# Optimization experiments

Hardware: AMD Instinct MI355X
Metric: run time of the kernel (lower is better)

The kernel has to match this reference:

```python
import jax, jax.numpy as jnp
import numpy as np
from jax import lax

ALPHA = 0.5
TEMPORAL_UNIT = 0


def setup_inputs() -> dict:
    key = jax.random.key(0)
    k1, k2, k3 = jax.random.split(key, 3)
    B, T, C = 16, 1024, 64
    z1 = jax.random.normal(k1, (B, T, C), dtype=jnp.float32)
    z2 = jax.random.normal(k2, (B, T, C), dtype=jnp.float32)
    # irregular timestamps, sorted within each sequence
    t = jnp.sort(jax.random.uniform(k3, (B, T), dtype=jnp.float32) * T, axis=1)
    return {"z1": z1, "z2": z2, "t": t}


def _instance_contrastive_loss_aug(z1, z2, t):
    B, T, C = z1.shape
    if B == 1:
        return jnp.asarray(0.0, z1.dtype)
    N = B * T
    tf = t.reshape(N)
    diff = jnp.abs(tf[:, None] - tf[None, :])                  # [N, N]
    seq = jnp.repeat(jnp.arange(B), T)                         # [N]
    same_seq = seq[:, None] == seq[None, :]
    # torch: diff[mask] += diff.max() + 0.001 (max of original diff)
    diff = jnp.where(same_seq, diff + (diff.max() + 0.001), diff)
    # B smallest per row -> top_k of negated values
    _, idx = lax.top_k(-diff, B)                               # [N, B]
    z1f = z1.reshape(N, C)
    z2f = z2.reshape(N, C)
    pos = jnp.sum(z1f * z2f, axis=-1, keepdims=True)           # [N, 1]
    neg11 = jnp.einsum('nc,nbc->nb', z1f, z1f[idx])            # [N, B]
    neg12 = jnp.einsum('nc,nbc->nb', z1f, z2f[idx])            # [N, B]
    logits = jnp.concatenate([pos, neg11, neg12], axis=1)      # [N, 1+2B]
    return -jax.nn.log_softmax(logits, axis=1)[:, 0].mean()


def _temporal_contrastive_loss(z1, z2):
    B, T, C = z1.shape
    if T == 1:
        return jnp.asarray(0.0, z1.dtype)
    z = jnp.concatenate([z1, z2], axis=1)                      # [B, 2T, C]
    sim = jnp.einsum('bic,bjc->bij', z, z)                     # [B, 2T, 2T]
    logits = jnp.tril(sim, -1)[:, :, :-1] + jnp.triu(sim, 1)[:, :, 1:]
    logp = jax.nn.log_softmax(logits, axis=-1)
    i = jnp.arange(T)
    return -(logp[:, i, T + i - 1].mean() + logp[:, T + i, i].mean()) / 2


def _hierarchical_loss(z1, z2, t, alpha, temporal_unit):
    B = z1.shape[0]
    loss = jnp.asarray(0.0, z1.dtype)
    d = 0
    while z1.shape[1] > 1:
        if alpha != 0:
            loss = loss + alpha * _instance_contrastive_loss_aug(z1, z2, t)
        if d >= temporal_unit and (1 - alpha) != 0:
            loss = loss + (1 - alpha) * _temporal_contrastive_loss(z1, z2)
        d += 1
        # pool timestamps by mean-of-2 (drop trailing odd element)
        if t.shape[1] % 2 != 0:
            t = t[:, :-1]
        t = t.reshape(B, -1, 2).mean(axis=2)
        # max_pool1d(kernel=2, stride=2) along time (floor -> truncate to even)
        Te = (z1.shape[1] // 2) * 2
        z1 = z1[:, :Te].reshape(B, -1, 2, z1.shape[-1]).max(axis=2)
        z2 = z2[:, :Te].reshape(B, -1, 2, z2.shape[-1]).max(axis=2)
    if z1.shape[1] == 1:
        if alpha != 0:
            loss = loss + alpha * _instance_contrastive_loss_aug(z1, z2, t)
        d += 1
    return loss / d


def reference(z1, z2, t):
    return _hierarchical_loss(z1, z2, t, ALPHA, TEMPORAL_UNIT)
```

## Files before the change

kernel.cpp:

```cpp
#include <hip/hip_runtime.h>
#include <hip/hip_bf16.h>
#include <math.h>

#define B_ 16
#define C_ 64
#define NEG_BIG (-1e30f)
#define POS_BIG (1e30f)

typedef __attribute__((ext_vector_type(8))) short bf16x8;
typedef __attribute__((ext_vector_type(4))) float f32x4;

__device__ __forceinline__ short f2bf(float x) {
  __hip_bfloat16 h = __float2bfloat16(x);
  return *reinterpret_cast<short*>(&h);
}

__device__ constexpr int kTS[10]   = {0, 512, 768, 896, 960, 992, 1008, 1024, 1040, 1056};
__device__ constexpr int kZOff[10] = {0, 2097152, 3145728, 3670016, 3932160, 4063232,
                                      4128768, 4161536, 4177920, 4186112};
__device__ constexpr int kIS[11] = {0, 256, 384, 448, 480, 496, 504, 508, 510, 511, 512};
__device__ constexpr int kO1[11] = {0, 0, 1056768, 1585152, 1849344, 1981440, 2047488,
                                    2080512, 2097024, 2105280, 2109408};
__device__ constexpr int kO2[11] = {0, 524288, 1318912, 1716224, 1914880, 2014208, 2063872,
                                    2088704, 2101120, 2107328, 2110432};
__device__ constexpr int kOT[11] = {0, 1048576, 1581056, 1847296, 1980416, 2046976, 2080256,
                                    2096896, 2105216, 2109376, 2111456};

__global__ __launch_bounds__(256) void convert0_kernel(
    const float* __restrict__ z1, const float* __restrict__ z2, short* __restrict__ zcb)
{
  int i = blockIdx.x * 256 + threadIdx.x;
  int n = i * 8;
  int b = n >> 16;
  float4 u1 = *(const float4*)(z1 + n), v1 = *(const float4*)(z1 + n + 4);
  float4 u2 = *(const float4*)(z2 + n), v2 = *(const float4*)(z2 + n + 4);
  bf16x8 f1, f2;
  f1[0]=f2bf(u1.x); f1[1]=f2bf(u1.y); f1[2]=f2bf(u1.z); f1[3]=f2bf(u1.w);
  f1[4]=f2bf(v1.x); f1[5]=f2bf(v1.y); f1[6]=f2bf(v1.z); f1[7]=f2bf(v1.w);
  f2[0]=f2bf(u2.x); f2[1]=f2bf(u2.y); f2[2]=f2bf(u2.z); f2[3]=f2bf(u2.w);
  f2[4]=f2bf(v2.x); f2[5]=f2bf(v2.y); f2[6]=f2bf(v2.z); f2[7]=f2bf(v2.w);
  *(bf16x8*)(zcb + (size_t)n + (size_t)b * 65536) = f1;
  *(bf16x8*)(zcb + (size_t)n + (size_t)(b + 1) * 65536) = f2;
}

__global__ __launch_bounds__(256) void downsample_kernel(
    const float* __restrict__ z1s, const float* __restrict__ z2s, const float* __restrict__ ts,
    float* __restrict__ z1d, float* __restrict__ z2d, float* __restrict__ td,
    short* __restrict__ zcb_l, int Td)
{
  int idx = blockIdx.x * blockDim.x + threadIdx.x;
  int total_z = B_ * Td * C_;
  if (idx < total_z) {
    int bi = idx >> 6;
    int b  = bi / Td;
    int s  = (b * (2 * Td) + 2 * (bi % Td)) * C_ + (idx & (C_ - 1));
    float v1 = fmaxf(z1s[s], z1s[s + C_]);
    float v2 = fmaxf(z2s[s], z2s[s + C_]);
    z1d[idx] = v1; z2d[idx] = v2;
    if (zcb_l) {
      int zi = idx + b * Td * C_;
      zcb_l[zi] = f2bf(v1);
      zcb_l[zi + Td * C_] = f2bf(v2);
    }
  } else {
    int k = idx - total_z;
    if (k < B_ * Td) {
      int i = k % Td, b = k / Td;
      int s = b * (2 * Td) + 2 * i;
      td[k] = 0.5f * (ts[s] + ts[s + 1]);
    }
  }
}

__global__ __launch_bounds__(256) void instance_fused(
    const float* __restrict__ z1_0, const float* __restrict__ z2_0, const float* __restrict__ t_0,
    const float* __restrict__ ws, float* __restrict__ out)
{
  __shared__ float dmin[64 * 17], dLl[64 * 17], dRl[64 * 17];
  __shared__ int   Lp[64 * 17], Rp[64 * 17];
  __shared__ int   nbrs[64][16];

  int bid = blockIdx.x;
  int l = 0, ls = 0;
  #pragma unroll
  for (int i = 1; i < 11; i++) if (bid >= kIS[i]) { l = i; ls = kIS[i]; }
  int T = 1024 >> l, lgT = 10 - l, N = B_ * T;
  const float *z1, *z2, *t;
  if (l == 0) { z1 = z1_0; z2 = z2_0; t = t_0; }
  else {
    int i1 = 0, i2 = 0, it = 0;
    #pragma unroll
    for (int i = 1; i < 11; i++) if (l == i) { i1 = kO1[i]; i2 = kO2[i]; it = kOT[i]; }
    z1 = ws + i1; z2 = ws + i2; t = ws + it;
  }
  float scale = 0.5f / (11.0f * (float)N);

  int tid = threadIdx.x;
  int rbase = (bid - ls) * 64;

  if (T == 1) {
    for (int idx = tid; idx < 64 * 16; idx += 256)
      nbrs[idx >> 4][idx & 15] = idx & 15;
  } else {
    for (int idx = tid; idx < 64 * 16; idx += 256) {
      int r = idx >> 4, s = idx & 15;
      int n = rbase + r;
      if (s < 15 && n < N) {
        int bq = n >> lgT;
        float q = t[n];
        int bs = s + (s >= bq ? 1 : 0);
        const float* tb = t + (bs << lgT);
        int li = 0;
        for (int k = T >> 1; k; k >>= 1) li += (tb[li + k - 1] < q) ? k : 0;
        li += (tb[li] < q) ? 1 : 0;
        float dl = (li >= 1) ? (q - tb[li - 1]) : POS_BIG;
        float dr = (li < T)  ? (tb[li] - q)     : POS_BIG;
        int o = r * 17 + s;
        Lp[o] = li - 1; Rp[o] = li;
        dLl[o] = dl; dRl[o] = dr; dmin[o] = fminf(dl, dr);
      }
    }
  }
  __syncthreads();

  int w = tid >> 6, lane = tid & 63;

  if (T > 1 && lane < 16) {
    int r = w * 16 + lane;
    int n = rbase + r;
    if (n < N) {
      int bq = n >> lgT;
      float q = t[n];
      #pragma unroll 1
      for (int j = 0; j < 16; j++) {
        float best = dmin[r * 17]; int sb = 0;
        #pragma unroll
        for (int s = 1; s < 15; s++) {
          float c = dmin[r * 17 + s];
          bool lt = c < best; best = lt ? c : best; sb = lt ? s : sb;
        }
        int o = r * 17 + sb;
        int bs = sb + (sb >= bq ? 1 : 0);
        float dl = dLl[o], dr = dRl[o];
        if (dl <= dr) {
          int p = Lp[o];
          nbrs[r][j] = bs * T + p;
          int pn = p - 1; Lp[o] = pn;
          float nd = (pn >= 0) ? (q - t[bs * T + pn]) : POS_BIG;
          dLl[o] = nd; dmin[o] = fminf(nd, dr);
        } else {
          int p = Rp[o];
          nbrs[r][j] = bs * T + p;
          int pn = p + 1; Rp[o] = pn;
          float nd = (pn < T) ? (t[bs * T + pn] - q) : POS_BIG;
          dRl[o] = nd; dmin[o] = fminf(dl, nd);
        }
      }
    } else {
      #pragma unroll
      for (int j = 0; j < 16; j++) nbrs[r][j] = 0;
    }
  }
  __syncthreads();

  int g = lane >> 4, sl = lane & 15;
  float loss = 0.f;
  #pragma unroll 1
  for (int rc = 0; rc < 4; rc++) {
    int r = w * 16 + rc * 4 + g;
    int n = rbase + r;
    bool act = n < N;
    int ns = act ? n : rbase;
    float4 za = *(const float4*)(z1 + (size_t)ns * C_ + sl * 4);
    float4 zp = *(const float4*)(z2 + (size_t)ns * C_ + sl * 4);
    float pos = za.x * zp.x + za.y * zp.y + za.z * zp.z + za.w * zp.w;
    float a11[16], a12[16];
    #pragma unroll
    for (int j = 0; j < 16; j++) {
      int nb = nbrs[r][j];
      float4 uu = *(const float4*)(z1 + (size_t)nb * C_ + sl * 4);
      float4 vv = *(const float4*)(z2 + (size_t)nb * C_ + sl * 4);
      a11[j] = za.x * uu.x + za.y * uu.y + za.z * uu.z + za.w * uu.w;
      a12[j] = za.x * vv.x + za.y * vv.y + za.z * vv.z + za.w * vv.w;
    }
    #pragma unroll
    for (int msk = 1; msk < 16; msk <<= 1) {
      pos += __shfl_xor(pos, msk, 16);
      #pragma unroll
      for (int j = 0; j < 16; j++) {
        a11[j] += __shfl_xor(a11[j], msk, 16);
        a12[j] += __shfl_xor(a12[j], msk, 16);
      }
    }
    if (sl == 0 && act) {
      float m = pos;
      #pragma unroll
      for (int j = 0; j < 16; j++) m = fmaxf(m, fmaxf(a11[j], a12[j]));
      float se = __expf(pos - m);
      #pragma unroll
      for (int j = 0; j < 16; j++) se += __expf(a11[j] - m) + __expf(a12[j] - m);
      loss += (m + __logf(se)) - pos;
    }
  }
  #pragma unroll
  for (int off = 32; off; off >>= 1) loss += __shfl_down(loss, off, 64);
  if (lane == 0) atomicAdd(out, loss * scale);
}

__global__ __launch_bounds__(256) void temporal_fused(
    const float* __restrict__ z1_0, const float* __restrict__ z2_0,
    const float* __restrict__ ws, const short* __restrict__ zcb, float* __restrict__ out)
{
  __shared__ __align__(16) short sb[64 * 64];

  int orig = blockIdx.x;
  int bid = (orig & 7) * 134 + (orig >> 3);

  int l = 0, ls = 0;
  #pragma unroll
  for (int i = 1; i < 10; i++) if (bid >= kTS[i]) { l = i; ls = kTS[i]; }
  int T = 1024 >> l, TT = 2 * T;
  int lb = bid - ls;
  int lg = (5 - l) > 0 ? (5 - l) : 0;
  int b = lb >> lg, rblk = lb & ((1 << lg) - 1);

  int zoff = 0, fo1 = 0, fo2 = 0;
  #pragma unroll
  for (int i = 1; i < 10; i++) if (l == i) { zoff = kZOff[i]; fo1 = kO1[i]; fo2 = kO2[i]; }
  const short* zl = zcb + zoff + (size_t)b * TT * C_;
  const float* z1b = ((l == 0) ? z1_0 : ws + fo1) + (size_t)b * T * C_;
  const float* z2b = ((l == 0) ? z2_0 : ws + fo2) + (size_t)b * T * C_;

  int tid = threadIdx.x;
  int wv = tid >> 6, lane = tid & 63, lo = lane & 15, hi = lane >> 4;
  int rowbase = rblk * 64 + wv * 16;
  bool activew = rowbase < TT;
  int diagch = rowbase >> 6;

  int ar = rowbase + lo; if (ar >= TT) ar = TT - 1;
  const short* pa = zl + (size_t)ar * C_;
  bf16x8 a0 = *(const bf16x8*)(pa + hi * 8);
  bf16x8 a1 = *(const bf16x8*)(pa + 32 + hi * 8);

  float m[4], s[4];
  #pragma unroll
  for (int sl = 0; sl < 4; sl++) { m[sl] = NEG_BIG; s[sl] = 0.f; }

  int c0 = tid, c1 = tid + 256;
  int r0 = c0 >> 3, s0 = c0 & 7, r1 = c1 >> 3, s1 = c1 & 7;
  int swb0 = r0 * 128 + ((s0 * 16) ^ ((r0 & 7) << 4));
  int swb1 = r1 * 128 + ((s1 * 16) ^ ((r1 & 7) << 4));

  int nch = (TT + 63) >> 6;
  int rr0 = r0, rr1 = r1;
  int q0 = rr0; if (q0 >= TT) q0 = TT - 1;
  int q1 = rr1; if (q1 >= TT) q1 = TT - 1;
  float4 st0 = *(const float4*)(zl + (size_t)q0 * C_ + s0 * 8);
  float4 st1 = *(const float4*)(zl + (size_t)q1 * C_ + s1 * 8);

  for (int ch = 0; ch < nch; ch++) {
    int cb = ch << 6;
    __syncthreads();
    *(float4*)((char*)sb + swb0) = st0;
    *(float4*)((char*)sb + swb1) = st1;
    __syncthreads();
    if (ch + 1 < nch) {
      int nb0 = cb + 64 + rr0; if (nb0 >= TT) nb0 = TT - 1;
      int nb1 = cb + 64 + rr1; if (nb1 >= TT) nb1 = TT - 1;
      st0 = *(const float4*)(zl + (size_t)nb0 * C_ + s0 * 8);
      st1 = *(const float4*)(zl + (size_t)nb1 * C_ + s1 * 8);
    }
    if (activew) {
      f32x4 acc[4];
      #pragma unroll
      for (int tt = 0; tt < 4; tt++) {
        int br = tt * 16 + lo;
        int byt = br * 128 + ((hi * 16) ^ ((br & 7) << 4));
        bf16x8 b0 = *(const bf16x8*)((const char*)sb + byt);
        bf16x8 b1 = *(const bf16x8*)((const char*)sb + (byt ^ 64));
        f32x4 c = {0.f, 0.f, 0.f, 0.f};
        c = __builtin_amdgcn_mfma_f32_16x16x32_bf16(a0, b0, c, 0, 0, 0);
        c = __builtin_amdgcn_mfma_f32_16x16x32_bf16(a1, b1, c, 0, 0, 0);
        acc[tt] = c;
      }
      bool maskpath = (ch == diagch) || (cb + 64 > TT);
      if (maskpath) {
        #pragma unroll
        for (int sl = 0; sl < 4; sl++) {
          int r = rowbase + hi * 4 + sl;
          float v[4]; float vmax = NEG_BIG;
          #pragma unroll
          for (int tt = 0; tt < 4; tt++) {
            int cg = cb + tt * 16 + lo;
            bool excl = (cg >= TT) || (cg == r);
            v[tt] = excl ? NEG_BIG : acc[tt][sl];
            vmax = fmaxf(vmax, v[tt]);
          }
          if (vmax > -1e29f) {
            float mn = fmaxf(m[sl], vmax);
            float ss = s[sl] * __expf(m[sl] - mn);
            #pragma unroll
            for (int tt = 0; tt < 4; tt++) ss += __expf(v[tt] - mn);
            s[sl] = ss; m[sl] = mn;
          }
        }
      } else {
        #pragma unroll
        for (int sl = 0; sl < 4; sl++) {
          float vmax = fmaxf(fmaxf(acc[0][sl], acc[1][sl]), fmaxf(acc[2][sl], acc[3][sl]));
          float mn = fmaxf(m[sl], vmax);
          float ss = s[sl] * __expf(m[sl] - mn);
          #pragma unroll
          for (int tt = 0; tt < 4; tt++) ss += __expf(acc[tt][sl] - mn);
          s[sl] = ss; m[sl] = mn;
        }
      }
    }
  }

  float pos[4] = {0.f, 0.f, 0.f, 0.f};
  if (activew) {
    #pragma unroll
    for (int sl = 0; sl < 4; sl++) {
      int r = rowbase + hi * 4 + sl;
      if (r < TT) {
        int rr = (r < T) ? r : r - T;
        float4 u = *(const float4*)(z1b + (size_t)rr * C_ + lo * 4);
        float4 v = *(const float4*)(z2b + (size_t)rr * C_ + lo * 4);
        pos[sl] = u.x * v.x + u.y * v.y + u.z * v.z + u.w * v.w;
      }
    }
  }

  #pragma unroll
  for (int msk = 1; msk < 16; msk <<= 1) {
    #pragma unroll
    for (int sl = 0; sl < 4; sl++) {
      float mo = __shfl_xor(m[sl], msk, 16);
      float so = __shfl_xor(s[sl], msk, 16);
      float po = __shfl_xor(pos[sl], msk, 16);
      float mn = fmaxf(m[sl], mo);
      s[sl] = s[sl] * __expf(m[sl] - mn) + so * __expf(mo - mn);
      m[sl] = mn;
      pos[sl] += po;
    }
  }

  float val = 0.f;
  if (lo == 0 && activew) {
    #pragma unroll
    for (int sl = 0; sl < 4; sl++) {
      int r = rowbase + hi * 4 + sl;
      if (r < TT) val += m[sl] + __logf(s[sl]) - pos[sl];
    }
  }
  #pragma unroll
  for (int off = 32; off; off >>= 1) val += __shfl_down(val, off, 64);
  float tscale = 0.5f / (11.0f * 2.0f * 16.0f * (float)T);
  if (lane == 0) atomicAdd(out, val * tscale);
}

extern "C" void kernel_launch(void* const* d_in, const int* in_sizes, int n_in,
                              void* d_out, int out_size, void* d_ws, size_t ws_size,
                              hipStream_t stream)
{
  (void)in_sizes; (void)n_in; (void)out_size; (void)ws_size;
  const float* z1_0 = (const float*)d_in[0];
  const float* z2_0 = (const float*)d_in[1];
  const float* t_0  = (const float*)d_in[2];
  float* out = (float*)d_out;
  float* ws  = (float*)d_ws;

  float* o1[11]; float* o2[11]; float* ot[11];
  size_t off = 0;
  for (int l = 1; l <= 10; l++) {
    int T = 1024 >> l;
    o1[l] = ws + off; off += (size_t)16 * T * 64;
    o2[l] = ws + off; off += (size_t)16 * T * 64;
    ot[l] = ws + off; off += (size_t)16 * T;
  }
  short* zcb = (short*)(ws + off);
  short* zl[10]; size_t zo = 0;
  for (int l = 0; l <= 9; l++) {
    zl[l] = zcb + zo; zo += (size_t)16 * 2 * (1024 >> l) * 64;
  }

  hipMemsetAsync(d_out, 0, sizeof(float), stream);

  hipLaunchKernelGGL(convert0_kernel, dim3(512), dim3(256), 0, stream, z1_0, z2_0, zl[0]);
  for (int l = 1; l <= 10; l++) {
    int T = 1024 >> l;
    int total = 16 * T * 64 + 16 * T;
    int blocks = (total + 255) / 256;
    hipLaunchKernelGGL(downsample_kernel, dim3(blocks), dim3(256), 0, stream,
                       (l == 1) ? z1_0 : o1[l - 1], (l == 1) ? z2_0 : o2[l - 1],
                       (l == 1) ? t_0 : ot[l - 1],
                       o1[l], o2[l], ot[l], (l <= 9) ? zl[l] : (short*)nullptr, T);
  }
  hipLaunchKernelGGL(instance_fused, dim3(513), dim3(256), 0, stream,
                     z1_0, z2_0, t_0, ws, out);
  hipLaunchKernelGGL(temporal_fused, dim3(1072), dim3(256), 0, stream,
                     z1_0, z2_0, ws, zcb, out);
}
```

Before: 162.2 us.

## Fuse pyramid downsampling into two kernels and drop LDS staging in temporal loss

Replaces the bf16 conversion kernel and ten per-level downsample launches with two kernels. The first computes levels 1-5 directly from the inputs via wider max/mean windows, and the second computes levels 6-10 from level 5. This is meant to cut launch count and serialization between levels, at the cost of redundant reads of the source data. The temporal kernel now loads B operands straight from global memory into registers with double buffering instead of staging through shared memory with barriers, lets idle waves exit early, and uses exp2 with pre-scaled log2e arithmetic.

New measurement: 242.5 us. +49.5%, slower.

```diff
diff --git a/kernel.cpp b/kernel.cpp
--- a/kernel.cpp
+++ b/kernel.cpp
@@ -6,6 +6,8 @@
 #define C_ 64
 #define NEG_BIG (-1e30f)
 #define POS_BIG (1e30f)
+#define L2E 1.44269504088896340736f
+#define LN2 0.69314718055994530942f
 
 typedef __attribute__((ext_vector_type(8))) short bf16x8;
 typedef __attribute__((ext_vector_type(4))) float f32x4;
@@ -26,49 +28,120 @@
 __device__ constexpr int kOT[11] = {0, 1048576, 1581056, 1847296, 1980416, 2046976, 2080256,
                                     2096896, 2105216, 2109376, 2111456};
 
-__global__ __launch_bounds__(256) void convert0_kernel(
-    const float* __restrict__ z1, const float* __restrict__ z2, short* __restrict__ zcb)
+__global__ __launch_bounds__(256) void pyramid1_kernel(
+    const float* __restrict__ z1, const float* __restrict__ z2, const float* __restrict__ t,
+    float* __restrict__ ws, short* __restrict__ zcb)
 {
-  int i = blockIdx.x * 256 + threadIdx.x;
-  int n = i * 8;
-  int b = n >> 16;
-  float4 u1 = *(const float4*)(z1 + n), v1 = *(const float4*)(z1 + n + 4);
-  float4 u2 = *(const float4*)(z2 + n), v2 = *(const float4*)(z2 + n + 4);
-  bf16x8 f1, f2;
-  f1[0]=f2bf(u1.x); f1[1]=f2bf(u1.y); f1[2]=f2bf(u1.z); f1[3]=f2bf(u1.w);
-  f1[4]=f2bf(v1.x); f1[5]=f2bf(v1.y); f1[6]=f2bf(v1.z); f1[7]=f2bf(v1.w);
-  f2[0]=f2bf(u2.x); f2[1]=f2bf(u2.y); f2[2]=f2bf(u2.z); f2[3]=f2bf(u2.w);
-  f2[4]=f2bf(v2.x); f2[5]=f2bf(v2.y); f2[6]=f2bf(v2.z); f2[7]=f2bf(v2.w);
-  *(bf16x8*)(zcb + (size_t)n + (size_t)b * 65536) = f1;
-  *(bf16x8*)(zcb + (size_t)n + (size_t)(b + 1) * 65536) = f2;
-}
-
-__global__ __launch_bounds__(256) void downsample_kernel(
-    const float* __restrict__ z1s, const float* __restrict__ z2s, const float* __restrict__ ts,
-    float* __restrict__ z1d, float* __restrict__ z2d, float* __restrict__ td,
-    short* __restrict__ zcb_l, int Td)
+  int idx = blockIdx.x * 256 + threadIdx.x;
+  if (idx < 131072) {
+    int n = idx * 8;
+    int b = n >> 16;
+    float4 u1 = *(const float4*)(z1 + n), v1 = *(const float4*)(z1 + n + 4);
+    float4 u2 = *(const float4*)(z2 + n), v2 = *(const float4*)(z2 + n + 4);
+    bf16x8 f1, f2;
+    f1[0]=f2bf(u1.x); f1[1]=f2bf(u1.y); f1[2]=f2bf(u1.z); f1[3]=f2bf(u1.w);
+    f1[4]=f2bf(v1.x); f1[5]=f2bf(v1.y); f1[6]=f2bf(v1.z); f1[7]=f2bf(v1.w);
+    f2[0]=f2bf(u2.x); f2[1]=f2bf(u2.y); f2[2]=f2bf(u2.z); f2[3]=f2bf(u2.w);
+    f2[4]=f2bf(v2.x); f2[5]=f2bf(v2.y); f2[6]=f2bf(v2.z); f2[7]=f2bf(v2.w);
+    *(bf16x8*)(zcb + (size_t)n + (size_t)b * 65536) = f1;
+    *(bf16x8*)(zcb + (size_t)n + (size_t)(b + 1) * 65536) = f2;
+  } else if (idx < 1146880) {
+    int li = idx - 131072;
+    int l = 1, st = 0;
+    if (li >= 524288) { l = 2; st = 524288; }
+    if (li >= 786432) { l = 3; st = 786432; }
+    if (li >= 917504) { l = 4; st = 917504; }
+    if (li >= 983040) { l = 5; st = 983040; }
+    int k = li - st;
+    int c = k & 63, bi = k >> 6;
+    int Tl = 1024 >> l;
+    int i = bi & (Tl - 1), b = bi >> (10 - l);
+    int w = 1 << l;
+    const float* p1 = z1 + ((((size_t)b << 10) + ((size_t)i << l)) << 6) + c;
+    const float* p2 = z2 + ((((size_t)b << 10) + ((size_t)i << l)) << 6) + c;
+    float m1 = p1[0], m2 = p2[0];
+    #pragma unroll 4
+    for (int j = 1; j < w; j++) { m1 = fmaxf(m1, p1[j << 6]); m2 = fmaxf(m2, p2[j << 6]); }
+    int o1 = 0, o2 = 0, zo = 0;
+    #pragma unroll
+    for (int q = 1; q <= 5; q++) if (l == q) { o1 = kO1[q]; o2 = kO2[q]; zo = kZOff[q]; }
+    ws[o1 + k] = m1; ws[o2 + k] = m2;
+    int zi = zo + ((b * 2 * Tl + i) << 6) + c;
+    zcb[zi] = f2bf(m1);
+    zcb[zi + (Tl << 6)] = f2bf(m2);
+  } else if (idx < 1162752) {
+    int kt = idx - 1146880;
+    int l = 1, st = 0;
+    if (kt >= 8192)  { l = 2; st = 8192; }
+    if (kt >= 12288) { l = 3; st = 12288; }
+    if (kt >= 14336) { l = 4; st = 14336; }
+    if (kt >= 15360) { l = 5; st = 15360; }
+    int k = kt - st;
+    int Tl = 1024 >> l;
+    int i = k & (Tl - 1), b = k >> (10 - l);
+    int w = 1 << l;
+    const float* pt = t + ((size_t)b << 10) + ((size_t)i << l);
+    float sum = 0.f;
+    #pragma unroll 4
+    for (int j = 0; j < w; j++) sum += pt[j];
+    int ot = 0;
+    #pragma unroll
+    for (int q = 1; q <= 5; q++) if (l == q) ot = kOT[q];
+    ws[ot + k] = sum / (float)w;
+  }
+}
+
+__global__ __launch_bounds__(256) void pyramid2_kernel(
+    float* __restrict__ ws, short* __restrict__ zcb)
 {
-  int idx = blockIdx.x * blockDim.x + threadIdx.x;
-  int total_z = B_ * Td * C_;
-  if (idx < total_z) {
-    int bi = idx >> 6;
-    int b  = bi / Td;
-    int s  = (b * (2 * Td) + 2 * (bi % Td)) * C_ + (idx & (C_ - 1));
-    float v1 = fmaxf(z1s[s], z1s[s + C_]);
-    float v2 = fmaxf(z2s[s], z2s[s + C_]);
-    z1d[idx] = v1; z2d[idx] = v2;
-    if (zcb_l) {
-      int zi = idx + b * Td * C_;
-      zcb_l[zi] = f2bf(v1);
-      zcb_l[zi + Td * C_] = f2bf(v2);
-    }
-  } else {
-    int k = idx - total_z;
-    if (k < B_ * Td) {
-      int i = k % Td, b = k / Td;
-      int s = b * (2 * Td) + 2 * i;
-      td[k] = 0.5f * (ts[s] + ts[s + 1]);
-    }
+  int idx = blockIdx.x * 256 + threadIdx.x;
+  const float* z15 = ws + kO1[5];
+  const float* z25 = ws + kO2[5];
+  const float* t5  = ws + kOT[5];
+  if (idx < 31744) {
+    int l = 6, st = 0;
+    if (idx >= 16384) { l = 7;  st = 16384; }
+    if (idx >= 24576) { l = 8;  st = 24576; }
+    if (idx >= 28672) { l = 9;  st = 28672; }
+    if (idx >= 30720) { l = 10; st = 30720; }
+    int k = idx - st;
+    int c = k & 63, bi = k >> 6;
+    int Tl = 1024 >> l;
+    int i = bi & (Tl - 1), b = bi >> (10 - l);
+    int w = 1 << (l - 5);
+    const float* p1 = z15 + ((((size_t)b << 5) + ((size_t)i << (l - 5))) << 6) + c;
+    const float* p2 = z25 + ((((size_t)b << 5) + ((size_t)i << (l - 5))) << 6) + c;
+    float m1 = p1[0], m2 = p2[0];
+    #pragma unroll 4
+    for (int j = 1; j < w; j++) { m1 = fmaxf(m1, p1[j << 6]); m2 = fmaxf(m2, p2[j << 6]); }
+    int o1 = 0, o2 = 0, zo = 0;
+    #pragma unroll
+    for (int q = 6; q <= 10; q++) if (l == q) { o1 = kO1[q]; o2 = kO2[q]; zo = (q <= 9) ? kZOff[q] : -1; }
+    ws[o1 + k] = m1; ws[o2 + k] = m2;
+    if (l <= 9) {
+      int zi = zo + ((b * 2 * Tl + i) << 6) + c;
+      zcb[zi] = f2bf(m1);
+      zcb[zi + (Tl << 6)] = f2bf(m2);
+    }
+  } else if (idx < 32240) {
+    int kt = idx - 31744;
+    int l = 6, st = 0;
+    if (kt >= 256) { l = 7;  st = 256; }
+    if (kt >= 384) { l = 8;  st = 384; }
+    if (kt >= 448) { l = 9;  st = 448; }
+    if (kt >= 480) { l = 10; st = 480; }
+    int k = kt - st;
+    int Tl = 1024 >> l;
+    int i = k & (Tl - 1), b = k >> (10 - l);
+    int w = 1 << (l - 5);
+    const float* pt = t5 + ((size_t)b << 5) + ((size_t)i << (l - 5));
+    float sum = 0.f;
+    #pragma unroll
+    for (int j = 0; j < w; j++) sum += pt[j];
+    int ot = 0;
+    #pragma unroll
+    for (int q = 6; q <= 10; q++) if (l == q) ot = kOT[q];
+    ws[ot + k] = sum / (float)w;
   }
 }
 
@@ -211,8 +284,6 @@
     const float* __restrict__ z1_0, const float* __restrict__ z2_0,
     const float* __restrict__ ws, const short* __restrict__ zcb, float* __restrict__ out)
 {
-  __shared__ __align__(16) short sb[64 * 64];
-
   int orig = blockIdx.x;
   int bid = (orig & 7) * 134 + (orig >> 3);
 
@@ -234,7 +305,7 @@
   int tid = threadIdx.x;
   int wv = tid >> 6, lane = tid & 63, lo = lane & 15, hi = lane >> 4;
   int rowbase = rblk * 64 + wv * 16;
-  bool activew = rowbase < TT;
+  if (rowbase >= TT) return;
   int diagch = rowbase >> 6;
 
   int ar = rowbase + lo; if (ar >= TT) ar = TT - 1;
@@ -242,116 +313,114 @@
   bf16x8 a0 = *(const bf16x8*)(pa + hi * 8);
   bf16x8 a1 = *(const bf16x8*)(pa + 32 + hi * 8);
 
-  float m[4], s[4];
-  #pragma unroll
-  for (int sl = 0; sl < 4; sl++) { m[sl] = NEG_BIG; s[sl] = 0.f; }
-
-  int c0 = tid, c1 = tid + 256;
-  int r0 = c0 >> 3, s0 = c0 & 7, r1 = c1 >> 3, s1 = c1 & 7;
-  int swb0 = r0 * 128 + ((s0 * 16) ^ ((r0 & 7) << 4));
-  int swb1 = r1 * 128 + ((s1 * 16) ^ ((r1 & 7) << 4));
+  float mb[4], s[4];
+  #pragma unroll
+  for (int q = 0; q < 4; q++) { mb[q] = NEG_BIG; s[q] = 0.f; }
 
   int nch = (TT + 63) >> 6;
-  int rr0 = r0, rr1 = r1;
-  int q0 = rr0; if (q0 >= TT) q0 = TT - 1;
-  int q1 = rr1; if (q1 >= TT) q1 = TT - 1;
-  float4 st0 = *(const float4*)(zl + (size_t)q0 * C_ + s0 * 8);
-  float4 st1 = *(const float4*)(zl + (size_t)q1 * C_ + s1 * 8);
-
-  for (int ch = 0; ch < nch; ch++) {
+
+  bf16x8 f0[4], f1[4], g0[4], g1[4];
+
+  auto loadB = [&](int ch, bf16x8 (&b0)[4], bf16x8 (&b1)[4]) {
     int cb = ch << 6;
-    __syncthreads();
-    *(float4*)((char*)sb + swb0) = st0;
-    *(float4*)((char*)sb + swb1) = st1;
-    __syncthreads();
-    if (ch + 1 < nch) {
-      int nb0 = cb + 64 + rr0; if (nb0 >= TT) nb0 = TT - 1;
-      int nb1 = cb + 64 + rr1; if (nb1 >= TT) nb1 = TT - 1;
-      st0 = *(const float4*)(zl + (size_t)nb0 * C_ + s0 * 8);
-      st1 = *(const float4*)(zl + (size_t)nb1 * C_ + s1 * 8);
-    }
-    if (activew) {
-      f32x4 acc[4];
-      #pragma unroll
-      for (int tt = 0; tt < 4; tt++) {
-        int br = tt * 16 + lo;
-        int byt = br * 128 + ((hi * 16) ^ ((br & 7) << 4));
-        bf16x8 b0 = *(const bf16x8*)((const char*)sb + byt);
-        bf16x8 b1 = *(const bf16x8*)((const char*)sb + (byt ^ 64));
-        f32x4 c = {0.f, 0.f, 0.f, 0.f};
-        c = __builtin_amdgcn_mfma_f32_16x16x32_bf16(a0, b0, c, 0, 0, 0);
-        c = __builtin_amdgcn_mfma_f32_16x16x32_bf16(a1, b1, c, 0, 0, 0);
-        acc[tt] = c;
-      }
-      bool maskpath = (ch == diagch) || (cb + 64 > TT);
-      if (maskpath) {
+    #pragma unroll
+    for (int tt = 0; tt < 4; tt++) {
+      int br = cb + tt * 16 + lo; if (br >= TT) br = TT - 1;
+      const short* pb = zl + (size_t)br * C_;
+      b0[tt] = *(const bf16x8*)(pb + hi * 8);
+      b1[tt] = *(const bf16x8*)(pb + 32 + hi * 8);
+    }
+  };
+
+  auto compute = [&](int ch, bf16x8 (&b0)[4], bf16x8 (&b1)[4]) {
+    int cb = ch << 6;
+    f32x4 acc[4];
+    #pragma unroll
+    for (int tt = 0; tt < 4; tt++) {
+      f32x4 c = {0.f, 0.f, 0.f, 0.f};
+      c = __builtin_amdgcn_mfma_f32_16x16x32_bf16(a0, b0[tt], c, 0, 0, 0);
+      c = __builtin_amdgcn_mfma_f32_16x16x32_bf16(a1, b1[tt], c, 0, 0, 0);
+      acc[tt] = c;
+    }
+    bool maskpath = (ch == diagch) || (cb + 64 > TT);
+    if (maskpath) {
+      #pragma unroll
+      for (int sl = 0; sl < 4; sl++) {
+        int r = rowbase + hi * 4 + sl;
+        float v[4]; float vmax = NEG_BIG;
         #pragma unroll
-        for (int sl = 0; sl < 4; sl++) {
-          int r = rowbase + hi * 4 + sl;
-          float v[4]; float vmax = NEG_BIG;
+        for (int tt = 0; tt < 4; tt++) {
+          int cg = cb + tt * 16 + lo;
+          bool excl = (cg >= TT) || (cg == r);
+          v[tt] = excl ? NEG_BIG : acc[tt][sl];
+          vmax = fmaxf(vmax, v[tt]);
+        }
+        if (vmax > -1e29f) {
+          float mn = fmaxf(mb[sl], vmax * L2E);
+          float ss = s[sl] * exp2f(mb[sl] - mn);
           #pragma unroll
-          for (int tt = 0; tt < 4; tt++) {
-            int cg = cb + tt * 16 + lo;
-            bool excl = (cg >= TT) || (cg == r);
-            v[tt] = excl ? NEG_BIG : acc[tt][sl];
-            vmax = fmaxf(vmax, v[tt]);
-          }
-          if (vmax > -1e29f) {
-            float mn = fmaxf(m[sl], vmax);
-            float ss = s[sl] * __expf(m[sl] - mn);
-            #pragma unroll
-            for (int tt = 0; tt < 4; tt++) ss += __expf(v[tt] - mn);
-            s[sl] = ss; m[sl] = mn;
-          }
-        }
-      } else {
-        #pragma unroll
-        for (int sl = 0; sl < 4; sl++) {
-          float vmax = fmaxf(fmaxf(acc[0][sl], acc[1][sl]), fmaxf(acc[2][sl], acc[3][sl]));
-          float mn = fmaxf(m[sl], vmax);
-          float ss = s[sl] * __expf(m[sl] - mn);
-          #pragma unroll
-          for (int tt = 0; tt < 4; tt++) ss += __expf(acc[tt][sl] - mn);
-          s[sl] = ss; m[sl] = mn;
+          for (int tt = 0; tt < 4; tt++) ss += exp2f(fmaf(v[tt], L2E, -mn));
+          s[sl] = ss; mb[sl] = mn;
         }
       }
-    }
+    } else {
+      #pragma unroll
+      for (int sl = 0; sl < 4; sl++) {
+        float vmax = fmaxf(fmaxf(acc[0][sl], acc[1][sl]), fmaxf(acc[2][sl], acc[3][sl]));
+        float mn = fmaxf(mb[sl], vmax * L2E);
+        float ss = s[sl] * exp2f(mb[sl] - mn);
+        #pragma unroll
+        for (int tt = 0; tt < 4; tt++) ss += exp2f(fmaf(acc[tt][sl], L2E, -mn));
+        s[sl] = ss; mb[sl] = mn;
+      }
+    }
+  };
+
+  loadB(0, f0, f1);
+  int ch = 0;
+  while (true) {
+    if (ch + 1 < nch) loadB(ch + 1, g0, g1);
+    compute(ch, f0, f1);
+    ch++;
+    if (ch >= nch) break;
+    if (ch + 1 < nch) loadB(ch + 1, f0, f1);
+    compute(ch, g0, g1);
+    ch++;
+    if (ch >= nch) break;
   }
 
   float pos[4] = {0.f, 0.f, 0.f, 0.f};
-  if (activew) {
+  #pragma unroll
+  for (int sl = 0; sl < 4; sl++) {
+    int r = rowbase + hi * 4 + sl;
+    if (r < TT) {
+      int rr = (r < T) ? r : r - T;
+      float4 u = *(const float4*)(z1b + (size_t)rr * C_ + lo * 4);
+      float4 v = *(const float4*)(z2b + (size_t)rr * C_ + lo * 4);
+      pos[sl] = u.x * v.x + u.y * v.y + u.z * v.z + u.w * v.w;
+    }
+  }
+
+  #pragma unroll
+  for (int msk = 1; msk < 16; msk <<= 1) {
+    #pragma unroll
+    for (int sl = 0; sl < 4; sl++) {
+      float mo = __shfl_xor(mb[sl], msk, 16);
+      float so = __shfl_xor(s[sl], msk, 16);
+      float po = __shfl_xor(pos[sl], msk, 16);
+      float mn = fmaxf(mb[sl], mo);
+      s[sl] = s[sl] * exp2f(mb[sl] - mn) + so * exp2f(mo - mn);
+      mb[sl] = mn;
+      pos[sl] += po;
+    }
+  }
+
+  float val = 0.f;
+  if (lo == 0) {
     #pragma unroll
     for (int sl = 0; sl < 4; sl++) {
       int r = rowbase + hi * 4 + sl;
-      if (r < TT) {
-        int rr = (r < T) ? r : r - T;
-        float4 u = *(const float4*)(z1b + (size_t)rr * C_ + lo * 4);
-        float4 v = *(const float4*)(z2b + (size_t)rr * C_ + lo * 4);
-        pos[sl] = u.x * v.x + u.y * v.y + u.z * v.z + u.w * v.w;
-      }
-    }
-  }
-
-  #pragma unroll
-  for (int msk = 1; msk < 16; msk <<= 1) {
-    #pragma unroll
-    for (int sl = 0; sl < 4; sl++) {
-      float mo = __shfl_xor(m[sl], msk, 16);
-      float so = __shfl_xor(s[sl], msk, 16);
-      float po = __shfl_xor(pos[sl], msk, 16);
-      float mn = fmaxf(m[sl], mo);
-      s[sl] = s[sl] * __expf(m[sl] - mn) + so * __expf(mo - mn);
-      m[sl] = mn;
-      pos[sl] += po;
-    }
-  }
-
-  float val = 0.f;
-  if (lo == 0 && activew) {
-    #pragma unroll
-    for (int sl = 0; sl < 4; sl++) {
-      int r = rowbase + hi * 4 + sl;
-      if (r < TT) val += m[sl] + __logf(s[sl]) - pos[sl];
+      if (r < TT) val += LN2 * (mb[sl] + __log2f(s[sl])) - pos[sl];
     }
   }
   #pragma unroll
@@ -371,32 +440,13 @@
   float* out = (float*)d_out;
   float* ws  = (float*)d_ws;
 
-  float* o1[11]; float* o2[11]; float* ot[11];
-  size_t off = 0;
-  for (int l = 1; l <= 10; l++) {
-    int T = 1024 >> l;
-    o1[l] = ws + off; off += (size_t)16 * T * 64;
-    o2[l] = ws + off; off += (size_t)16 * T * 64;
-    ot[l] = ws + off; off += (size_t)16 * T;
-  }
-  short* zcb = (short*)(ws + off);
-  short* zl[10]; size_t zo = 0;
-  for (int l = 0; l <= 9; l++) {
-    zl[l] = zcb + zo; zo += (size_t)16 * 2 * (1024 >> l) * 64;
-  }
+  short* zcb = (short*)(ws + 2111472);
 
   hipMemsetAsync(d_out, 0, sizeof(float), stream);
 
-  hipLaunchKernelGGL(convert0_kernel, dim3(512), dim3(256), 0, stream, z1_0, z2_0, zl[0]);
-  for (int l = 1; l <= 10; l++) {
-    int T = 1024 >> l;
-    int total = 16 * T * 64 + 16 * T;
-    int blocks = (total + 255) / 256;
-    hipLaunchKernelGGL(downsample_kernel, dim3(blocks), dim3(256), 0, stream,
-                       (l == 1) ? z1_0 : o1[l - 1], (l == 1) ? z2_0 : o2[l - 1],
-                       (l == 1) ? t_0 : ot[l - 1],
-                       o1[l], o2[l], ot[l], (l <= 9) ? zl[l] : (short*)nullptr, T);
-  }
+  hipLaunchKernelGGL(pyramid1_kernel, dim3(4542), dim3(256), 0, stream,
+                     z1_0, z2_0, t_0, ws, zcb);
+  hipLaunchKernelGGL(pyramid2_kernel, dim3(126), dim3(256), 0, stream, ws, zcb);
   hipLaunchKernelGGL(instance_fused, dim3(513), dim3(256), 0, stream,
                      z1_0, z2_0, t_0, ws, out);
   hipLaunchKernelGGL(temporal_fused, dim3(1072), dim3(256), 0, stream,
```
